# Kernel optimization log

Hardware: AMD Instinct MI355X
Metric: run time of the kernel (lower is better)

## Reference

```python
import jax, jax.numpy as jnp
import numpy as np

NEG = 0.01   # LeakyReLU negative slope
EPS = 1e-5   # GraphNorm eps


def _graph_conv(x, src, dst, W):
    """DGL GraphConv, norm='both', no bias. x: [B,N,F], src/dst: [B,E], W: [F,H]."""
    B, N, _ = x.shape
    bidx = jnp.arange(B)[:, None]                      # [B,1] broadcast with [B,E]
    ones = jnp.ones(src.shape, x.dtype)
    out_deg = jnp.zeros((B, N), x.dtype).at[bidx, src].add(ones)
    in_deg = jnp.zeros((B, N), x.dtype).at[bidx, dst].add(ones)
    h = x @ W                                          # linear commutes with sum-aggregation
    h = h * jnp.maximum(out_deg, 1.0)[..., None] ** -0.5
    agg = jnp.zeros_like(h).at[bidx, dst].add(h[bidx, src])   # SpMM: scatter-add messages
    return agg * jnp.maximum(in_deg, 1.0)[..., None] ** -0.5


def _graph_norm(x, gamma, beta, alpha):
    """GraphNorm: per-graph, per-channel stats with learnable mean scale alpha."""
    mean = x.mean(axis=1, keepdims=True)               # [B,1,H]
    sub = x - alpha * mean
    var = (sub * sub).mean(axis=1, keepdims=True)
    return gamma * sub * jax.lax.rsqrt(var + EPS) + beta


def _universal_readout(x, W1, b1, W2, b2):
    """Per-node MLP (H -> H/2 -> H/4) then unweighted mean over nodes."""
    h = jax.nn.relu(x @ W1 + b1)
    return (h @ W2 + b2).mean(axis=1)                  # [B, H/4]


def _weighted_mean(x, w, ar):
    """dgl.mean_nodes with weights: mean over nodes of (w_i * ar_i) * x_i."""
    return ((w * ar)[..., None] * x).mean(axis=1)      # [B, F]


def setup_inputs() -> dict:
    key = jax.random.key(0)
    B, N, E, F, H = 2048, 50, 500, 64, 256
    ks = jax.random.split(key, 24)
    s = 0.05
    inp = {
        "node_feats": jax.random.normal(ks[0], (B, N, F), jnp.float32),
        "weights": jax.random.uniform(ks[1], (B, N), jnp.float32),
        "src": jax.random.randint(ks[2], (B, E), 0, N, jnp.int32),
        "dst": jax.random.randint(ks[3], (B, E), 0, N, jnp.int32),
        "W1": jax.random.normal(ks[4], (F, H), jnp.float32) * s,
        "W2": jax.random.normal(ks[5], (H, H), jnp.float32) * s,
        "W3": jax.random.normal(ks[6], (H, H), jnp.float32) * s,
        "ar1": jnp.ones((N,), jnp.float32),
        "ar2": jnp.ones((N,), jnp.float32),
        "ar3": jnp.ones((N,), jnp.float32),
        "ar4": jnp.ones((N,), jnp.float32),
    }
    for i in range(3):
        inp[f"gn{i+1}_gamma"] = jnp.ones((H,), jnp.float32)
        inp[f"gn{i+1}_beta"] = jnp.zeros((H,), jnp.float32)
        inp[f"gn{i+1}_alpha"] = jnp.ones((H,), jnp.float32)
        inp[f"r{i+1}_W1"] = jax.random.normal(ks[7 + 4 * i], (H, H // 2), jnp.float32) * s
        inp[f"r{i+1}_b1"] = jnp.zeros((H // 2,), jnp.float32)
        inp[f"r{i+1}_W2"] = jax.random.normal(ks[8 + 4 * i], (H // 2, H // 4), jnp.float32) * s
        inp[f"r{i+1}_b2"] = jnp.zeros((H // 4,), jnp.float32)
    return inp


def reference(node_feats, weights, src, dst, W1, W2, W3,
              ar1, ar2, ar3, ar4,
              gn1_gamma, gn1_beta, gn1_alpha,
              gn2_gamma, gn2_beta, gn2_alpha,
              gn3_gamma, gn3_beta, gn3_alpha,
              r1_W1, r1_b1, r1_W2, r1_b2,
              r2_W1, r2_b1, r2_W2, r2_b2,
              r3_W1, r3_b1, r3_W2, r3_b2):
    lrelu = lambda x: jax.nn.leaky_relu(x, NEG)
    parts = [_weighted_mean(node_feats, weights, ar1)]
    h = lrelu(_graph_norm(_graph_conv(node_feats, src, dst, W1), gn1_gamma, gn1_beta, gn1_alpha))
    parts += [_universal_readout(h, r1_W1, r1_b1, r1_W2, r1_b2), _weighted_mean(h, weights, ar2)]
    h = lrelu(_graph_norm(_graph_conv(h, src, dst, W2), gn2_gamma, gn2_beta, gn2_alpha))
    parts += [_universal_readout(h, r2_W1, r2_b1, r2_W2, r2_b2), _weighted_mean(h, weights, ar3)]
    h = lrelu(_graph_norm(_graph_conv(h, src, dst, W3), gn3_gamma, gn3_beta, gn3_alpha))
    parts += [_universal_readout(h, r3_W1, r3_b1, r3_W2, r3_b2), _weighted_mean(h, weights, ar4)]
    return lrelu(jnp.concatenate(parts, axis=-1))    # [B, 64 + 3*(64+256)] = [B, 1024]
```

## Files before the change

### kernel.cpp

```cpp
#include <hip/hip_runtime.h>

#define NEG 0.01f

typedef float f32x4 __attribute__((ext_vector_type(4)));
typedef short short8 __attribute__((ext_vector_type(8)));

__device__ __forceinline__ float lrelu(float v) { return v > 0.f ? v : NEG * v; }

__device__ __forceinline__ unsigned short bf16_rne(float x) {
  unsigned u = __float_as_uint(x);
  unsigned r = u + 0x7fffu + ((u >> 16) & 1u);
  return (unsigned short)(r >> 16);
}
__device__ __forceinline__ float bf16_to_f(unsigned short h) {
  return __uint_as_float(((unsigned)h) << 16);
}

#define MFMA16(a, b, c) __builtin_amdgcn_mfma_f32_16x16x32_bf16(a, b, c, 0, 0, 0)

__global__ void prep_planes(const float* __restrict__ W1, const float* __restrict__ W2,
                            const float* __restrict__ W3, const float* __restrict__ R1,
                            const float* __restrict__ R2, const float* __restrict__ R3,
                            unsigned short* __restrict__ ws) {
  int idx = blockIdx.x * 256 + threadIdx.x;
  if (idx >= 245760) return;
  const float* src; int K, N; unsigned short *hi, *lo; int e;
  if (idx < 16384)       { src = W1; K = 64;  N = 256; hi = ws;          lo = ws + 16384;  e = idx; }
  else if (idx < 81920)  { src = W2; K = 256; N = 256; hi = ws + 32768;  lo = ws + 98304;  e = idx - 16384; }
  else if (idx < 147456) { src = W3; K = 256; N = 256; hi = ws + 163840; lo = ws + 229376; e = idx - 81920; }
  else if (idx < 180224) { src = R1; K = 256; N = 128; hi = ws + 294912; lo = ws + 327680; e = idx - 147456; }
  else if (idx < 212992) { src = R2; K = 256; N = 128; hi = ws + 360448; lo = ws + 393216; e = idx - 180224; }
  else                   { src = R3; K = 256; N = 128; hi = ws + 425984; lo = ws + 458752; e = idx - 212992; }
  int n = e / K, k = e - n * K;
  float v = src[k * N + n];
  unsigned short hb = bf16_rne(v);
  hi[e] = hb;
  lo[e] = bf16_rne(v - bf16_to_f(hb));
}

template <int KK>
__device__ __forceinline__ void conv_mfma(const char* AhiB, const char* AloB,
                                          const unsigned short* __restrict__ Whi,
                                          const unsigned short* __restrict__ Wlo,
                                          f32x4 acc[4][2], int w, int l) {
  const int g = l >> 4, r15 = l & 15;
  const int aswz = (l & 7) << 4;
  const int arow = r15 << 9;
  const int colA = w * 32 + r15;
#pragma unroll
  for (int kt = 0; kt < KK / 32; ++kt) {
    const int ka = (kt * 64 + g * 16) ^ aswz;
    const int ke = kt * 32 + g * 8;
    short8 ah[4], al[4];
#pragma unroll
    for (int mt = 0; mt < 4; ++mt) {
      ah[mt] = *(const short8*)(AhiB + (mt * 8192 + arow + ka));
      al[mt] = *(const short8*)(AloB + (mt * 8192 + arow + ka));
    }
#pragma unroll
    for (int nt = 0; nt < 2; ++nt) {
      const int wc = colA + nt * 16;
      short8 bh = *(const short8*)(Whi + (size_t)wc * KK + ke);
      short8 bl = *(const short8*)(Wlo + (size_t)wc * KK + ke);
#pragma unroll
      for (int mt = 0; mt < 4; ++mt) {
        acc[mt][nt] = MFMA16(ah[mt], bh, acc[mt][nt]);
        acc[mt][nt] = MFMA16(al[mt], bh, acc[mt][nt]);
        acc[mt][nt] = MFMA16(ah[mt], bl, acc[mt][nt]);
      }
    }
  }
}

__device__ __forceinline__ void mlp1_mfma(const char* AhiB, const char* AloB,
                                          const unsigned short* __restrict__ Whi,
                                          const unsigned short* __restrict__ Wlo,
                                          const float* __restrict__ b1, float* s1sum,
                                          int w, int l) {
  const int g = l >> 4, r15 = l & 15;
  const int aswz = (l & 7) << 4;
  const int arow = r15 << 9;
  const int col = w * 16 + r15;
  f32x4 acc[4] = {};
#pragma unroll
  for (int kt = 0; kt < 8; ++kt) {
    const int ka = (kt * 64 + g * 16) ^ aswz;
    const int ke = kt * 32 + g * 8;
    short8 bh = *(const short8*)(Whi + (size_t)col * 256 + ke);
    short8 bl = *(const short8*)(Wlo + (size_t)col * 256 + ke);
#pragma unroll
    for (int mt = 0; mt < 4; ++mt) {
      short8 ah = *(const short8*)(AhiB + (mt * 8192 + arow + ka));
      short8 al = *(const short8*)(AloB + (mt * 8192 + arow + ka));
      acc[mt] = MFMA16(ah, bh, acc[mt]);
      acc[mt] = MFMA16(al, bh, acc[mt]);
      acc[mt] = MFMA16(ah, bl, acc[mt]);
    }
  }
  const float b1v = b1[col];
  float colsum = 0.f;
#pragma unroll
  for (int mt = 0; mt < 4; ++mt)
#pragma unroll
    for (int r = 0; r < 4; ++r) {
      float v = fmaxf(acc[mt][r] + b1v, 0.f);
      if (mt < 3) colsum += v;
      else if (g == 0 && r < 2) colsum += v;
    }
  colsum += __shfl_xor(colsum, 16);
  colsum += __shfl_xor(colsum, 32);
  if (l < 16) s1sum[w * 16 + l] = colsum;
}

struct GnnArgs {
  const float* x;  const float* w;  const int* src;  const int* dst;
  const float* ar[4];
  const float* gamma[3]; const float* beta[3]; const float* alpha[3];
  const float* rb1[3]; const float* rW2[3]; const float* rb2[3];
  const unsigned short* whi[3]; const unsigned short* wlo[3];
  const unsigned short* rhi[3]; const unsigned short* rlo[3];
};

template <int KK>
__device__ __forceinline__ void do_layer(
    char* AhiB, char* AloB, float* Cchunk, float* agg,
    const unsigned short* csr_s, const int* rs,
    const float* w_lds, float* war, const float* outs_, const float* ins_,
    float* statsS1, float* statsS2, float* wmacc, float* s1sum,
    const unsigned short* Whi, const unsigned short* Wlo,
    const unsigned short* Rhi, const unsigned short* Rlo,
    const float* gamma, const float* beta, const float* alpha,
    const float* ar_next, const float* b1, const float* rW2f, const float* b2,
    float* out, int b, int ro_off, int t, int w, int l) {
  f32x4 acc[4][2] = {};
  conv_mfma<KK>(AhiB, AloB, Whi, Wlo, acc, w, l);

  const int g = l >> 4, r15 = l & 15;
#pragma unroll 1
  for (int ch = 0; ch < 4; ++ch) {
    __syncthreads();
    if (t < 64) statsS1[t] = 0.f;
    else if (t < 128) statsS2[t - 64] = 0.f;
    if (ch == 0) {
      if (t < 256) wmacc[t] = 0.f;
      if (t < 50) war[t] = w_lds[t] * ar_next[t];
    }
    if ((w >> 1) == ch) {
      const int cb = (w & 1) * 32;
#pragma unroll
      for (int mt = 0; mt < 4; ++mt)
#pragma unroll
        for (int nt = 0; nt < 2; ++nt)
#pragma unroll
          for (int r = 0; r < 4; ++r) {
            int row = mt * 16 + g * 4 + r;
            if (row < 50)
              Cchunk[row * 64 + cb + nt * 16 + r15] = acc[mt][nt][r] * outs_[row];
          }
    }
    __syncthreads();
    {
      const int lo2 = l & 31, hf = l >> 5;
      for (int d = w; d < 50; d += 8) {
        float ax = 0.f, ay = 0.f;
        const int e1 = rs[d + 1];
        for (int e = rs[d] + hf; e < e1; e += 2) {
          int s = csr_s[e];
          const float2 cv = *(const float2*)&Cchunk[s * 64 + lo2 * 2];
          ax += cv.x; ay += cv.y;
        }
        ax += __shfl_xor(ax, 32);
        ay += __shfl_xor(ay, 32);
        if (hf == 0) { agg[d * 64 + lo2 * 2] = ax; agg[d * 64 + lo2 * 2 + 1] = ay; }
      }
    }
    __syncthreads();
    {
      const int c = t & 63;
      float s1 = 0.f, s2 = 0.f;
      for (int j = 0; j < 7; ++j) {
        int n = (t >> 6) + 8 * j;
        if (n < 50) { float v = agg[n * 64 + c] * ins_[n]; s1 += v; s2 += v * v; }
      }
      atomicAdd(&statsS1[c], s1);
      atomicAdd(&statsS2[c], s2);
    }
    __syncthreads();
    {
      const int c = t & 63, colg = ch * 64 + c;
      const float m = statsS1[c] * 0.02f;
      const float am = alpha[colg] * m;
      const float varr = statsS2[c] * 0.02f - am * (2.f * m - am);
      const float gi = gamma[colg] * rsqrtf(fmaxf(varr, 0.f) + 1e-5f);
      const float be = beta[colg];
      float wmp = 0.f;
      for (int j = 0; j < 7; ++j) {
        int n = (t >> 6) + 8 * j;
        if (n < 50) {
          float v = agg[n * 64 + c] * ins_[n];
          float o = (v - am) * gi + be;
          o = o > 0.f ? o : NEG * o;
          wmp += war[n] * o;
          unsigned short hb = bf16_rne(o);
          float resid = o - bf16_to_f(hb);
          int bo = (n * 512 + 2 * colg) ^ ((n & 7) << 4);
          *(unsigned short*)(AhiB + bo) = hb;
          *(unsigned short*)(AloB + bo) = bf16_rne(resid);
        }
      }
      atomicAdd(&wmacc[colg], wmp);
    }
  }
  __syncthreads();
  mlp1_mfma(AhiB, AloB, Rhi, Rlo, b1, s1sum, w, l);
  __syncthreads();
  if (t < 64) {
    float a = 0.f;
    for (int k = 0; k < 128; ++k) a += s1sum[k] * rW2f[k * 64 + t];
    a = a * 0.02f + b2[t];
    out[b * 1024 + ro_off + t] = lrelu(a);
  }
  if (t < 256) out[b * 1024 + ro_off + 64 + t] = lrelu(wmacc[t] * 0.02f);
}

__global__ __launch_bounds__(512, 4) void gnn_fused(GnnArgs a, float* __restrict__ out) {
  __shared__ alignas(16) char bigb[76800];
  char* AhiB   = bigb;
  char* AloB   = bigb + 25600;
  float* Cchunk = (float*)(bigb + 51200);
  float* agg    = (float*)(bigb + 64000);
  __shared__ alignas(16) char smallb[4864];
  unsigned short* csr_s = (unsigned short*)smallb;
  int*   rs      = (int*)(smallb + 1024);
  int*   cnt     = (int*)(smallb + 1280);
  float* w_lds   = (float*)(smallb + 1792);
  float* war     = (float*)(smallb + 2048);
  float* outs_   = (float*)(smallb + 2304);
  float* ins_    = (float*)(smallb + 2560);
  float* statsS1 = (float*)(smallb + 2816);
  float* statsS2 = (float*)(smallb + 3072);
  float* wmacc   = (float*)(smallb + 3328);
  float* s1sum   = (float*)(smallb + 4352);
  int* fillp = (int*)statsS1;

  const int t = threadIdx.x, b = blockIdx.x;
  const int l = t & 63, w = t >> 6;

  if (t < 128) cnt[t] = 0;
  if (t < 64) fillp[t] = 0;
  if (t < 256) wmacc[t] = 0.f;
  if (t < 50) w_lds[t] = a.w[b * 50 + t];
  __syncthreads();
  int es = 0, ed = 0;
  if (t < 500) {
    es = a.src[b * 500 + t];
    ed = a.dst[b * 500 + t];
    atomicAdd(&cnt[es], 1);
    atomicAdd(&cnt[64 + ed], 1);
  }
  __syncthreads();
  if (t < 50) {
    outs_[t] = rsqrtf(fmaxf((float)cnt[t], 1.f));
    ins_[t]  = rsqrtf(fmaxf((float)cnt[64 + t], 1.f));
    war[t] = w_lds[t] * a.ar[0][t];
  }
  if (t == 0) {
    int run = 0;
    for (int n = 0; n < 50; ++n) { rs[n] = run; run += cnt[64 + n]; }
    rs[50] = run;
  }
  __syncthreads();
  if (t < 500) {
    int pos = rs[ed] + atomicAdd(&fillp[ed], 1);
    csr_s[pos] = (unsigned short)es;
  }
  {
    const int c = t & 63;
    float wmp = 0.f;
    for (int j = 0; j < 7; ++j) {
      int n = (t >> 6) + 8 * j;
      if (n < 50) {
        float v = a.x[b * 3200 + n * 64 + c];
        wmp += war[n] * v;
        unsigned short hb = bf16_rne(v);
        float resid = v - bf16_to_f(hb);
        int bo = (n * 512 + 2 * c) ^ ((n & 7) << 4);
        *(unsigned short*)(AhiB + bo) = hb;
        *(unsigned short*)(AloB + bo) = bf16_rne(resid);
      }
    }
    atomicAdd(&wmacc[c], wmp);
  }
  __syncthreads();
  if (t < 64) out[b * 1024 + t] = lrelu(wmacc[t] * 0.02f);

  do_layer<64>(AhiB, AloB, Cchunk, agg, csr_s, rs, w_lds, war, outs_, ins_,
               statsS1, statsS2, wmacc, s1sum,
               a.whi[0], a.wlo[0], a.rhi[0], a.rlo[0],
               a.gamma[0], a.beta[0], a.alpha[0], a.ar[1],
               a.rb1[0], a.rW2[0], a.rb2[0], out, b, 64, t, w, l);
  do_layer<256>(AhiB, AloB, Cchunk, agg, csr_s, rs, w_lds, war, outs_, ins_,
                statsS1, statsS2, wmacc, s1sum,
                a.whi[1], a.wlo[1], a.rhi[1], a.rlo[1],
                a.gamma[1], a.beta[1], a.alpha[1], a.ar[2],
                a.rb1[1], a.rW2[1], a.rb2[1], out, b, 384, t, w, l);
  do_layer<256>(AhiB, AloB, Cchunk, agg, csr_s, rs, w_lds, war, outs_, ins_,
                statsS1, statsS2, wmacc, s1sum,
                a.whi[2], a.wlo[2], a.rhi[2], a.rlo[2],
                a.gamma[2], a.beta[2], a.alpha[2], a.ar[3],
                a.rb1[2], a.rW2[2], a.rb2[2], out, b, 704, t, w, l);
}

extern "C" void kernel_launch(void* const* d_in, const int* in_sizes, int n_in,
                              void* d_out, int out_size, void* d_ws, size_t ws_size,
                              hipStream_t stream) {
  const float* W1 = (const float*)d_in[4];
  const float* W2 = (const float*)d_in[5];
  const float* W3 = (const float*)d_in[6];
  const float* R1 = (const float*)d_in[14];
  const float* R2 = (const float*)d_in[21];
  const float* R3 = (const float*)d_in[28];
  unsigned short* ws = (unsigned short*)d_ws;

  hipLaunchKernelGGL(prep_planes, dim3(960), dim3(256), 0, stream,
                     W1, W2, W3, R1, R2, R3, ws);

  GnnArgs a;
  a.x = (const float*)d_in[0];
  a.w = (const float*)d_in[1];
  a.src = (const int*)d_in[2];
  a.dst = (const int*)d_in[3];
  a.ar[0] = (const float*)d_in[7];
  a.ar[1] = (const float*)d_in[8];
  a.ar[2] = (const float*)d_in[9];
  a.ar[3] = (const float*)d_in[10];
  for (int i = 0; i < 3; ++i) {
    a.gamma[i] = (const float*)d_in[11 + 7 * i];
    a.beta[i]  = (const float*)d_in[12 + 7 * i];
    a.alpha[i] = (const float*)d_in[13 + 7 * i];
    a.rb1[i]   = (const float*)d_in[15 + 7 * i];
    a.rW2[i]   = (const float*)d_in[16 + 7 * i];
    a.rb2[i]   = (const float*)d_in[17 + 7 * i];
  }
  a.whi[0] = ws;          a.wlo[0] = ws + 16384;
  a.whi[1] = ws + 32768;  a.wlo[1] = ws + 98304;
  a.whi[2] = ws + 163840; a.wlo[2] = ws + 229376;
  a.rhi[0] = ws + 294912; a.rlo[0] = ws + 327680;
  a.rhi[1] = ws + 360448; a.rlo[1] = ws + 393216;
  a.rhi[2] = ws + 425984; a.rlo[2] = ws + 458752;

  const int B = in_sizes[0] / 3200;
  hipLaunchKernelGGL(gnn_fused, dim3(B), dim3(512), 0, stream, a, (float*)d_out);
}
```

Before: 858.6 us.

## Tile weight planes for coalesced MFMA B loads and vectorize SpMM gather

Weight hi/lo bf16 planes are stored pre-tiled in 16x8 blocks, so each lane's B-fragment load becomes a contiguous 128-element chunk instead of a strided column read. The Cchunk LDS buffer gets an XOR swizzle, and the SpMM gather now uses float4 reads with 4-way edge splitting. In-degree scaling and GraphNorm statistics accumulation are folded into the aggregation loop, which removes one barrier phase but adds more LDS atomics. Launch bounds drop from 4 to 2 blocks per SM, which loosens register limits at the cost of possible occupancy.

```diff
diff --git a/kernel.cpp b/kernel.cpp
--- a/kernel.cpp
+++ b/kernel.cpp
@@ -32,10 +32,11 @@
   else if (idx < 212992) { src = R2; K = 256; N = 128; hi = ws + 360448; lo = ws + 393216; e = idx - 180224; }
   else                   { src = R3; K = 256; N = 128; hi = ws + 425984; lo = ws + 458752; e = idx - 212992; }
   int n = e / K, k = e - n * K;
+  int dst = ((n >> 4) * (K >> 3) + (k >> 3)) * 128 + (n & 15) * 8 + (k & 7);
   float v = src[k * N + n];
   unsigned short hb = bf16_rne(v);
-  hi[e] = hb;
-  lo[e] = bf16_rne(v - bf16_to_f(hb));
+  hi[dst] = hb;
+  lo[dst] = bf16_rne(v - bf16_to_f(hb));
 }
 
 template <int KK>
@@ -46,11 +47,9 @@
   const int g = l >> 4, r15 = l & 15;
   const int aswz = (l & 7) << 4;
   const int arow = r15 << 9;
-  const int colA = w * 32 + r15;
 #pragma unroll
   for (int kt = 0; kt < KK / 32; ++kt) {
     const int ka = (kt * 64 + g * 16) ^ aswz;
-    const int ke = kt * 32 + g * 8;
     short8 ah[4], al[4];
 #pragma unroll
     for (int mt = 0; mt < 4; ++mt) {
@@ -59,9 +58,9 @@
     }
 #pragma unroll
     for (int nt = 0; nt < 2; ++nt) {
-      const int wc = colA + nt * 16;
-      short8 bh = *(const short8*)(Whi + (size_t)wc * KK + ke);
-      short8 bl = *(const short8*)(Wlo + (size_t)wc * KK + ke);
+      const size_t bo = ((size_t)(w * 2 + nt) * (KK >> 3) + kt * 4 + g) * 128 + r15 * 8;
+      short8 bh = *(const short8*)(Whi + bo);
+      short8 bl = *(const short8*)(Wlo + bo);
 #pragma unroll
       for (int mt = 0; mt < 4; ++mt) {
         acc[mt][nt] = MFMA16(ah[mt], bh, acc[mt][nt]);
@@ -85,9 +84,9 @@
 #pragma unroll
   for (int kt = 0; kt < 8; ++kt) {
     const int ka = (kt * 64 + g * 16) ^ aswz;
-    const int ke = kt * 32 + g * 8;
-    short8 bh = *(const short8*)(Whi + (size_t)col * 256 + ke);
-    short8 bl = *(const short8*)(Wlo + (size_t)col * 256 + ke);
+    const size_t bo = ((size_t)w * 32 + kt * 4 + g) * 128 + r15 * 8;
+    short8 bh = *(const short8*)(Whi + bo);
+    short8 bl = *(const short8*)(Wlo + bo);
 #pragma unroll
     for (int mt = 0; mt < 4; ++mt) {
       short8 ah = *(const short8*)(AhiB + (mt * 8192 + arow + ka));
@@ -154,36 +153,40 @@
 #pragma unroll
           for (int r = 0; r < 4; ++r) {
             int row = mt * 16 + g * 4 + r;
-            if (row < 50)
-              Cchunk[row * 64 + cb + nt * 16 + r15] = acc[mt][nt][r] * outs_[row];
+            if (row < 50) {
+              int c = cb + nt * 16 + r15;
+              int cp = ((((c >> 2) ^ (row & 7)) << 2) | (c & 3));
+              Cchunk[row * 64 + cp] = acc[mt][nt][r] * outs_[row];
+            }
           }
     }
     __syncthreads();
     {
-      const int lo2 = l & 31, hf = l >> 5;
+      const int lo4 = l & 15, hf = l >> 4;
       for (int d = w; d < 50; d += 8) {
-        float ax = 0.f, ay = 0.f;
+        f32x4 v = {0.f, 0.f, 0.f, 0.f};
         const int e1 = rs[d + 1];
-        for (int e = rs[d] + hf; e < e1; e += 2) {
+        for (int e = rs[d] + hf; e < e1; e += 4) {
           int s = csr_s[e];
-          const float2 cv = *(const float2*)&Cchunk[s * 64 + lo2 * 2];
-          ax += cv.x; ay += cv.y;
+          const f32x4 cv = *(const f32x4*)&Cchunk[s * 64 + ((lo4 ^ (s & 7)) << 2)];
+          v += cv;
         }
-        ax += __shfl_xor(ax, 32);
-        ay += __shfl_xor(ay, 32);
-        if (hf == 0) { agg[d * 64 + lo2 * 2] = ax; agg[d * 64 + lo2 * 2 + 1] = ay; }
+#pragma unroll
+        for (int j = 0; j < 4; ++j) {
+          v[j] += __shfl_xor(v[j], 16);
+          v[j] += __shfl_xor(v[j], 32);
+        }
+        if (hf == 0) {
+          const float is = ins_[d];
+          f32x4 sv = v * is;
+          *(f32x4*)&agg[d * 64 + lo4 * 4] = sv;
+#pragma unroll
+          for (int j = 0; j < 4; ++j) {
+            atomicAdd(&statsS1[lo4 * 4 + j], sv[j]);
+            atomicAdd(&statsS2[lo4 * 4 + j], sv[j] * sv[j]);
+          }
+        }
       }
-    }
-    __syncthreads();
-    {
-      const int c = t & 63;
-      float s1 = 0.f, s2 = 0.f;
-      for (int j = 0; j < 7; ++j) {
-        int n = (t >> 6) + 8 * j;
-        if (n < 50) { float v = agg[n * 64 + c] * ins_[n]; s1 += v; s2 += v * v; }
-      }
-      atomicAdd(&statsS1[c], s1);
-      atomicAdd(&statsS2[c], s2);
     }
     __syncthreads();
     {
@@ -197,7 +200,7 @@
       for (int j = 0; j < 7; ++j) {
         int n = (t >> 6) + 8 * j;
         if (n < 50) {
-          float v = agg[n * 64 + c] * ins_[n];
+          float v = agg[n * 64 + c];
           float o = (v - am) * gi + be;
           o = o > 0.f ? o : NEG * o;
           wmp += war[n] * o;
@@ -223,7 +226,7 @@
   if (t < 256) out[b * 1024 + ro_off + 64 + t] = lrelu(wmacc[t] * 0.02f);
 }
 
-__global__ __launch_bounds__(512, 4) void gnn_fused(GnnArgs a, float* __restrict__ out) {
+__global__ __launch_bounds__(512, 2) void gnn_fused(GnnArgs a, float* __restrict__ out) {
   __shared__ alignas(16) char bigb[76800];
   char* AhiB   = bigb;
   char* AloB   = bigb + 25600;
```

Result: slower. 1.474 ms (+71.7%).
